# Kernel optimization log

Measured on AMD Instinct MI355X. Metric: run time of the kernel, lower is better.

## Reference

```python
import jax, jax.numpy as jnp
import numpy as np

B, N, D = 256, 512, 128   # meta_batch, num_sample, feat_dim; in_c = 2*D = 256, base_c = 128
EPS_L1 = 1e-12
EPS_BN = 1e-5
NEG_SLOPE = 0.01


def setup_inputs() -> dict:
    key = jax.random.key(0)
    ks = jax.random.split(key, 6)
    return {
        "distribution_edge": jax.random.uniform(ks[0], (B, N, N), dtype=jnp.float32),
        "instance_edge": jax.random.uniform(ks[1], (B, N, N), dtype=jnp.float32),
        "point_node": jax.random.normal(ks[2], (B, N, D), dtype=jnp.float32),
        "W1": jax.random.normal(ks[3], (2 * D, 2 * D), dtype=jnp.float32) * 0.05,  # Conv2d 1x1: (out_c=base_c*2, in_c)
        "g1": jnp.ones((2 * D,), jnp.float32),
        "b1": jnp.zeros((2 * D,), jnp.float32),
        "W2": jax.random.normal(ks[4], (D, 2 * D), dtype=jnp.float32) * 0.05,     # Conv2d 1x1: (out_c=base_c, base_c*2)
        "g2": jnp.ones((D,), jnp.float32),
        "b2": jnp.zeros((D,), jnp.float32),
    }


def _l1_normalize(x):
    # F.normalize(x, p=1, dim=-1): x / max(sum(|x|, -1), 1e-12)
    return x / jnp.clip(jnp.sum(jnp.abs(x), axis=-1, keepdims=True), EPS_L1, None)


def _bn_lrelu(x, g, b):
    # x: (B, C, N); BatchNorm2d training-mode stats over (batch, spatial), biased var
    mean = jnp.mean(x, axis=(0, 2), keepdims=True)
    var = jnp.var(x, axis=(0, 2), keepdims=True)
    y = (x - mean) * jax.lax.rsqrt(var + EPS_BN) * g[None, :, None] + b[None, :, None]
    return jnp.where(y >= 0, y, NEG_SLOPE * y)


def reference(distribution_edge, instance_edge, point_node, W1, g1, b1, W2, g2, b2):
    n = point_node.shape[1]
    diag_mask = 1.0 - jnp.eye(n, dtype=point_node.dtype)  # broadcasts over meta_batch
    edge_feat = _l1_normalize(distribution_edge * diag_mask)
    aggr_feat = jnp.einsum('bij,bjd->bid', edge_feat, point_node)
    edge_instance = _l1_normalize(instance_edge * diag_mask)
    aggr_instance = jnp.einsum('bij,bjd->bid', edge_instance, point_node)
    x = jnp.concatenate([aggr_feat, aggr_instance], axis=-1)  # (B, N, 2D)
    x = jnp.swapaxes(x, 1, 2)                                  # (B, 2D, N)
    h = _bn_lrelu(jnp.einsum('oc,bcn->bon', W1, x), g1, b1)    # 1x1 conv, no bias
    h = _bn_lrelu(jnp.einsum('oc,bcn->bon', W2, h), g2, b2)
    return jnp.swapaxes(h, 1, 2)                               # (B, N, base_c)
```

## Files before the change

kernel.cpp:

```cpp
#include <hip/hip_runtime.h>
#include <hip/hip_bf16.h>
#include <string.h>

#define BB 256
#define NNS 512
#define DDF 128
#define CC1 256
#define CC2 128
#define NPOS (BB * NNS)

typedef __attribute__((ext_vector_type(4))) float f32x4;
typedef __attribute__((ext_vector_type(8))) short bf16x8;

__device__ __forceinline__ short f2bf(float f) {
    __hip_bfloat16 h = __float2bfloat16(f);
    short s;
    __builtin_memcpy(&s, &h, 2);
    return s;
}
__device__ __forceinline__ float bf2f(short s) {
    unsigned int u = ((unsigned int)(unsigned short)s) << 16;
    float f;
    __builtin_memcpy(&f, &u, 4);
    return f;
}

#define MFMA16(a, b, c) __builtin_amdgcn_mfma_f32_16x16x32_bf16(a, b, c, 0, 0, 0)

__global__ void prep_kernel(const float* __restrict__ W1, const float* __restrict__ W2,
                            short* __restrict__ W1b, short* __restrict__ W2b,
                            float* __restrict__ stats) {
    int idx = blockIdx.x * 256 + threadIdx.x;
    if (idx < CC1 * CC1) W1b[idx] = f2bf(W1[idx]);
    if (idx < CC2 * CC1) W2b[idx] = f2bf(W2[idx]);
    if (idx < 1536) stats[idx] = 0.0f;
}

__global__ void transposeP_kernel(const float* __restrict__ P, short* __restrict__ PT) {
    int oid = blockIdx.x * 256 + threadIdx.x;
    int b = oid >> 13;
    int r = oid & 8191;
    int jo = r >> 7;
    int d = r & 127;
    const float* p = P + (size_t)b * (NNS * DDF) + (size_t)(jo * 8) * DDF + d;
    bf16x8 v;
#pragma unroll
    for (int t = 0; t < 8; ++t) v[t] = f2bf(p[t * DDF]);
    *reinterpret_cast<bf16x8*>(PT + ((size_t)(b * DDF + d)) * NNS + jo * 8) = v;
}

__global__ __launch_bounds__(256) void gemm1_kernel(const float* __restrict__ dE,
                                                    const float* __restrict__ iE,
                                                    const short* __restrict__ PT,
                                                    short* __restrict__ X) {
    int bid = blockIdx.x;
    int mtb = bid & 3;
    int e = (bid >> 2) & 1;
    int b = bid >> 3;
    const float* E = (e == 0 ? dE : iE) + (size_t)b * (NNS * NNS);
    const short* PTb = PT + (size_t)b * (DDF * NNS);

    int tid = threadIdx.x;
    int lane = tid & 63, w = tid >> 6;
    int quad = lane >> 4, lr = lane & 15;
    int mh = w >> 1, nh = w & 1;
    int mbase = mtb * 128 + mh * 64;

    f32x4 zero = {0.f, 0.f, 0.f, 0.f};
    f32x4 acc[4][4];
#pragma unroll
    for (int a = 0; a < 4; ++a)
#pragma unroll
        for (int c = 0; c < 4; ++c) acc[a][c] = zero;
    float rs[4] = {0.f, 0.f, 0.f, 0.f};

    for (int kk = 0; kk < 16; ++kk) {
        int k0 = kk * 32 + quad * 8;
        bf16x8 bfr[4];
#pragma unroll
        for (int nt = 0; nt < 4; ++nt) {
            int n = nh * 64 + nt * 16 + lr;
            bfr[nt] = *reinterpret_cast<const bf16x8*>(&PTb[(size_t)n * NNS + k0]);
        }
#pragma unroll
        for (int mt = 0; mt < 4; ++mt) {
            int i = mbase + mt * 16 + lr;
            const float* rp = &E[(size_t)i * NNS + k0];
            float4 v0 = *reinterpret_cast<const float4*>(rp);
            float4 v1 = *reinterpret_cast<const float4*>(rp + 4);
            float a8[8] = {v0.x, v0.y, v0.z, v0.w, v1.x, v1.y, v1.z, v1.w};
#pragma unroll
            for (int t = 0; t < 8; ++t)
                if (k0 + t == i) a8[t] = 0.0f;
#pragma unroll
            for (int t = 0; t < 8; ++t) rs[mt] += fabsf(a8[t]);
            bf16x8 af;
#pragma unroll
            for (int t = 0; t < 8; ++t) af[t] = f2bf(a8[t]);
#pragma unroll
            for (int nt = 0; nt < 4; ++nt) acc[mt][nt] = MFMA16(af, bfr[nt], acc[mt][nt]);
        }
    }

    float inv[4];
#pragma unroll
    for (int mt = 0; mt < 4; ++mt) {
        float s = rs[mt];
        s += __shfl_xor(s, 16, 64);
        s += __shfl_xor(s, 32, 64);
        inv[mt] = 1.0f / fmaxf(s, 1e-12f);
    }
#pragma unroll
    for (int mt = 0; mt < 4; ++mt) {
        float ir[4];
#pragma unroll
        for (int r = 0; r < 4; ++r) ir[r] = __shfl(inv[mt], quad * 4 + r, 64);
#pragma unroll
        for (int nt = 0; nt < 4; ++nt) {
            int col = e * 128 + nh * 64 + nt * 16 + lr;
#pragma unroll
            for (int r = 0; r < 4; ++r) {
                int row = mbase + mt * 16 + quad * 4 + r;
                X[((size_t)b * NNS + row) * CC1 + col] = f2bf(acc[mt][nt][r] * ir[r]);
            }
        }
    }
}

__global__ __launch_bounds__(256) void gemm2_kernel(const short* __restrict__ X,
                                                    const short* __restrict__ W1b,
                                                    short* __restrict__ Y1,
                                                    float* __restrict__ sum1,
                                                    float* __restrict__ sumsq1) {
    int bid = blockIdx.x;
    int ocb = (bid & 1) * 128;
    int pt = bid >> 1;
    int tid = threadIdx.x;
    int lane = tid & 63, w = tid >> 6;
    int quad = lane >> 4, lr = lane & 15;
    int mh = w >> 1, nh = w & 1;
    int pbase = pt * 128 + mh * 64;

    f32x4 zero = {0.f, 0.f, 0.f, 0.f};
    f32x4 acc[4][4];
#pragma unroll
    for (int a = 0; a < 4; ++a)
#pragma unroll
        for (int c = 0; c < 4; ++c) acc[a][c] = zero;

    for (int kk = 0; kk < 8; ++kk) {
        int k0 = kk * 32 + quad * 8;
        bf16x8 bfr[4];
#pragma unroll
        for (int nt = 0; nt < 4; ++nt) {
            int o = ocb + nh * 64 + nt * 16 + lr;
            bfr[nt] = *reinterpret_cast<const bf16x8*>(&W1b[(size_t)o * CC1 + k0]);
        }
#pragma unroll
        for (int mt = 0; mt < 4; ++mt) {
            int pos = pbase + mt * 16 + lr;
            bf16x8 af = *reinterpret_cast<const bf16x8*>(&X[(size_t)pos * CC1 + k0]);
#pragma unroll
            for (int nt = 0; nt < 4; ++nt) acc[mt][nt] = MFMA16(af, bfr[nt], acc[mt][nt]);
        }
    }
#pragma unroll
    for (int nt = 0; nt < 4; ++nt) {
        int o = ocb + nh * 64 + nt * 16 + lr;
        float s = 0.f, q = 0.f;
#pragma unroll
        for (int mt = 0; mt < 4; ++mt)
#pragma unroll
            for (int r = 0; r < 4; ++r) {
                float v = acc[mt][nt][r];
                s += v;
                q += v * v;
            }
        s += __shfl_xor(s, 16, 64); s += __shfl_xor(s, 32, 64);
        q += __shfl_xor(q, 16, 64); q += __shfl_xor(q, 32, 64);
        if (lane < 16) {
            atomicAdd(&sum1[o], s);
            atomicAdd(&sumsq1[o], q);
        }
#pragma unroll
        for (int mt = 0; mt < 4; ++mt)
#pragma unroll
            for (int r = 0; r < 4; ++r) {
                int pos = pbase + mt * 16 + quad * 4 + r;
                Y1[(size_t)pos * CC1 + o] = f2bf(acc[mt][nt][r]);
            }
    }
}

__global__ void finalize_kernel(const float* __restrict__ sum, const float* __restrict__ sumsq,
                                const float* __restrict__ g, const float* __restrict__ b,
                                float* __restrict__ scale, float* __restrict__ shift, int C) {
    int i = threadIdx.x;
    if (i < C) {
        const float invM = 1.0f / (float)NPOS;
        float m = sum[i] * invM;
        float v = sumsq[i] * invM - m * m;
        float s = g[i] * rsqrtf(v + 1e-5f);
        scale[i] = s;
        shift[i] = b[i] - m * s;
    }
}

__global__ __launch_bounds__(256) void gemm3_kernel(const short* __restrict__ Y1,
                                                    const short* __restrict__ W2b,
                                                    const float* __restrict__ scale1,
                                                    const float* __restrict__ shift1,
                                                    float* __restrict__ Y2,
                                                    float* __restrict__ sum2,
                                                    float* __restrict__ sumsq2) {
    __shared__ __align__(16) float ssc[CC1];
    __shared__ __align__(16) float ssh[CC1];
    ssc[threadIdx.x] = scale1[threadIdx.x];
    ssh[threadIdx.x] = shift1[threadIdx.x];
    __syncthreads();

    int pt = blockIdx.x;
    int tid = threadIdx.x;
    int lane = tid & 63, w = tid >> 6;
    int quad = lane >> 4, lr = lane & 15;
    int mh = w >> 1, nh = w & 1;
    int pbase = pt * 128 + mh * 64;

    f32x4 zero = {0.f, 0.f, 0.f, 0.f};
    f32x4 acc[4][4];
#pragma unroll
    for (int a = 0; a < 4; ++a)
#pragma unroll
        for (int c = 0; c < 4; ++c) acc[a][c] = zero;

    for (int kk = 0; kk < 8; ++kk) {
        int k0 = kk * 32 + quad * 8;
        bf16x8 bfr[4];
#pragma unroll
        for (int nt = 0; nt < 4; ++nt) {
            int o = nh * 64 + nt * 16 + lr;
            bfr[nt] = *reinterpret_cast<const bf16x8*>(&W2b[(size_t)o * CC1 + k0]);
        }
        float4 sc0 = *reinterpret_cast<const float4*>(&ssc[k0]);
        float4 sc1 = *reinterpret_cast<const float4*>(&ssc[k0 + 4]);
        float4 sh0 = *reinterpret_cast<const float4*>(&ssh[k0]);
        float4 sh1 = *reinterpret_cast<const float4*>(&ssh[k0 + 4]);
        float scv[8] = {sc0.x, sc0.y, sc0.z, sc0.w, sc1.x, sc1.y, sc1.z, sc1.w};
        float shv[8] = {sh0.x, sh0.y, sh0.z, sh0.w, sh1.x, sh1.y, sh1.z, sh1.w};
#pragma unroll
        for (int mt = 0; mt < 4; ++mt) {
            int pos = pbase + mt * 16 + lr;
            bf16x8 raw = *reinterpret_cast<const bf16x8*>(&Y1[(size_t)pos * CC1 + k0]);
            bf16x8 af;
#pragma unroll
            for (int t = 0; t < 8; ++t) {
                float v = bf2f(raw[t]) * scv[t] + shv[t];
                v = fmaxf(v, 0.01f * v);
                af[t] = f2bf(v);
            }
#pragma unroll
            for (int nt = 0; nt < 4; ++nt) acc[mt][nt] = MFMA16(af, bfr[nt], acc[mt][nt]);
        }
    }
#pragma unroll
    for (int nt = 0; nt < 4; ++nt) {
        int o = nh * 64 + nt * 16 + lr;
        float s = 0.f, q = 0.f;
#pragma unroll
        for (int mt = 0; mt < 4; ++mt)
#pragma unroll
            for (int r = 0; r < 4; ++r) {
                float v = acc[mt][nt][r];
                s += v;
                q += v * v;
            }
        s += __shfl_xor(s, 16, 64); s += __shfl_xor(s, 32, 64);
        q += __shfl_xor(q, 16, 64); q += __shfl_xor(q, 32, 64);
        if (lane < 16) {
            atomicAdd(&sum2[o], s);
            atomicAdd(&sumsq2[o], q);
        }
#pragma unroll
        for (int mt = 0; mt < 4; ++mt)
#pragma unroll
            for (int r = 0; r < 4; ++r) {
                int pos = pbase + mt * 16 + quad * 4 + r;
                Y2[(size_t)pos * CC2 + o] = acc[mt][nt][r];
            }
    }
}

__global__ void apply2_kernel(const float* __restrict__ Y2, const float* __restrict__ scale2,
                              const float* __restrict__ shift2, float* __restrict__ out) {
    size_t gid = (size_t)blockIdx.x * 256 + threadIdx.x;
    size_t base = gid * 4;
    float4 y = *reinterpret_cast<const float4*>(&Y2[base]);
    int o = (int)(base & 127);
    float4 sc = *reinterpret_cast<const float4*>(&scale2[o]);
    float4 sh = *reinterpret_cast<const float4*>(&shift2[o]);
    float4 t;
    t.x = y.x * sc.x + sh.x; t.x = fmaxf(t.x, 0.01f * t.x);
    t.y = y.y * sc.y + sh.y; t.y = fmaxf(t.y, 0.01f * t.y);
    t.z = y.z * sc.z + sh.z; t.z = fmaxf(t.z, 0.01f * t.z);
    t.w = y.w * sc.w + sh.w; t.w = fmaxf(t.w, 0.01f * t.w);
    *reinterpret_cast<float4*>(&out[base]) = t;
}

extern "C" void kernel_launch(void* const* d_in, const int* in_sizes, int n_in,
                              void* d_out, int out_size, void* d_ws, size_t ws_size,
                              hipStream_t stream) {
    const float* dE = (const float*)d_in[0];
    const float* iE = (const float*)d_in[1];
    const float* P  = (const float*)d_in[2];
    const float* W1 = (const float*)d_in[3];
    const float* g1 = (const float*)d_in[4];
    const float* b1 = (const float*)d_in[5];
    const float* W2 = (const float*)d_in[6];
    const float* g2 = (const float*)d_in[7];
    const float* b2 = (const float*)d_in[8];
    float* out = (float*)d_out;
    char* ws = (char*)d_ws;

    short* PT  = (short*)(ws + 0);
    short* X   = (short*)(ws + 33554432);
    short* Y1  = (short*)(ws + 100663296);
    float* Y2  = (float*)(ws + 33554432);
    short* W1b = (short*)(ws + 167772160);
    short* W2b = (short*)(ws + 167903232);
    float* st  = (float*)(ws + 167968768);
    float* sum1 = st,        * sumsq1 = st + 256, * scale1 = st + 512,  * shift1 = st + 768;
    float* sum2 = st + 1024, * sumsq2 = st + 1152, * scale2 = st + 1280, * shift2 = st + 1408;

    prep_kernel<<<256, 256, 0, stream>>>(W1, W2, W1b, W2b, st);
    transposeP_kernel<<<8192, 256, 0, stream>>>(P, PT);
    gemm1_kernel<<<2048, 256, 0, stream>>>(dE, iE, PT, X);
    gemm2_kernel<<<2048, 256, 0, stream>>>(X, W1b, Y1, sum1, sumsq1);
    finalize_kernel<<<1, 256, 0, stream>>>(sum1, sumsq1, g1, b1, scale1, shift1, CC1);
    gemm3_kernel<<<1024, 256, 0, stream>>>(Y1, W2b, scale1, shift1, Y2, sum2, sumsq2);
    finalize_kernel<<<1, 128, 0, stream>>>(sum2, sumsq2, g2, b2, scale2, shift2, CC2);
    apply2_kernel<<<16384, 256, 0, stream>>>(Y2, scale2, shift2, out);
}
```

Before: 893.8 us.

## Stage GEMM A-tiles through LDS with async global_load_lds double buffering

The three GEMM kernels now stream their A operand (edge rows, X, Y1) into XOR-swizzled shared memory with direct global-to-LDS loads, double-buffered across k-steps. Previously each wave read these rows straight from global memory in a strided pattern. The P transpose now goes through an LDS tile so global reads are coalesced. gemm2 moves to 512-thread blocks that cover all 256 output channels, so X is read once per tile instead of twice, and bf16 packing uses paired conversions. The cost is added LDS use and a barrier on every k-step.

```diff
diff --git a/kernel.cpp b/kernel.cpp
--- a/kernel.cpp
+++ b/kernel.cpp
@@ -23,6 +23,19 @@
     float f;
     __builtin_memcpy(&f, &u, 4);
     return f;
+}
+__device__ __forceinline__ unsigned int pk2bf(float a, float b) {
+    float2 t; t.x = a; t.y = b;
+    __hip_bfloat162 h = __float22bfloat162_rn(t);
+    unsigned int u;
+    __builtin_memcpy(&u, &h, 4);
+    return u;
+}
+
+__device__ __forceinline__ void gload_lds16(const void* g, void* l) {
+    __builtin_amdgcn_global_load_lds(
+        (const __attribute__((address_space(1))) unsigned int*)g,
+        (__attribute__((address_space(3))) unsigned int*)l, 16, 0, 0);
 }
 
 #define MFMA16(a, b, c) __builtin_amdgcn_mfma_f32_16x16x32_bf16(a, b, c, 0, 0, 0)
@@ -36,23 +49,37 @@
     if (idx < 1536) stats[idx] = 0.0f;
 }
 
-__global__ void transposeP_kernel(const float* __restrict__ P, short* __restrict__ PT) {
-    int oid = blockIdx.x * 256 + threadIdx.x;
-    int b = oid >> 13;
-    int r = oid & 8191;
-    int jo = r >> 7;
-    int d = r & 127;
-    const float* p = P + (size_t)b * (NNS * DDF) + (size_t)(jo * 8) * DDF + d;
-    bf16x8 v;
-#pragma unroll
-    for (int t = 0; t < 8; ++t) v[t] = f2bf(p[t * DDF]);
-    *reinterpret_cast<bf16x8*>(PT + ((size_t)(b * DDF + d)) * NNS + jo * 8) = v;
+__global__ __launch_bounds__(256) void transposeP_kernel(const float* __restrict__ P,
+                                                         short* __restrict__ PT) {
+    __shared__ float tp[64 * 132];
+    int b = blockIdx.x >> 3;
+    int j0 = (blockIdx.x & 7) * 64;
+    int t = threadIdx.x;
+    const float* Pb = P + ((size_t)b * NNS + j0) * DDF;
+    int jr = t >> 5, dc = (t & 31) * 4;
+#pragma unroll
+    for (int p = 0; p < 8; ++p) {
+        int j = p * 8 + jr;
+        float4 v = *reinterpret_cast<const float4*>(&Pb[(size_t)j * DDF + dc]);
+        *reinterpret_cast<float4*>(&tp[j * 132 + dc]) = v;
+    }
+    __syncthreads();
+    int jo = t & 7;
+#pragma unroll
+    for (int p = 0; p < 4; ++p) {
+        int d = p * 32 + (t >> 3);
+        bf16x8 v;
+#pragma unroll
+        for (int s = 0; s < 8; ++s) v[s] = f2bf(tp[(jo * 8 + s) * 132 + d]);
+        *reinterpret_cast<bf16x8*>(&PT[((size_t)(b * DDF + d)) * NNS + j0 + jo * 8]) = v;
+    }
 }
 
 __global__ __launch_bounds__(256) void gemm1_kernel(const float* __restrict__ dE,
                                                     const float* __restrict__ iE,
                                                     const short* __restrict__ PT,
                                                     short* __restrict__ X) {
+    __shared__ __align__(16) float tA[2][4096];
     int bid = blockIdx.x;
     int mtb = bid & 3;
     int e = (bid >> 2) & 1;
@@ -64,7 +91,16 @@
     int lane = tid & 63, w = tid >> 6;
     int quad = lane >> 4, lr = lane & 15;
     int mh = w >> 1, nh = w & 1;
-    int mbase = mtb * 128 + mh * 64;
+    int mbase = mtb * 128;
+    int mwave = mh * 64;
+
+    int srow[4], scol[4];
+#pragma unroll
+    for (int i = 0; i < 4; ++i) {
+        int rl = i * 32 + (tid >> 3);
+        srow[i] = rl;
+        scol[i] = (tid & 7) ^ (rl & 7);
+    }
 
     f32x4 zero = {0.f, 0.f, 0.f, 0.f};
     f32x4 acc[4][4];
@@ -74,7 +110,22 @@
         for (int c = 0; c < 4; ++c) acc[a][c] = zero;
     float rs[4] = {0.f, 0.f, 0.f, 0.f};
 
+#pragma unroll
+    for (int i = 0; i < 4; ++i)
+        gload_lds16(&E[(size_t)(mbase + srow[i]) * NNS + scol[i] * 4],
+                    (char*)&tA[0][0] + i * 4096 + w * 1024);
+    __syncthreads();
+
     for (int kk = 0; kk < 16; ++kk) {
+        const float* cur = &tA[kk & 1][0];
+        if (kk < 15) {
+            float* nxt = &tA[(kk + 1) & 1][0];
+            int kc = (kk + 1) * 32;
+#pragma unroll
+            for (int i = 0; i < 4; ++i)
+                gload_lds16(&E[(size_t)(mbase + srow[i]) * NNS + kc + scol[i] * 4],
+                            (char*)nxt + i * 4096 + w * 1024);
+        }
         int k0 = kk * 32 + quad * 8;
         bf16x8 bfr[4];
 #pragma unroll
@@ -84,22 +135,26 @@
         }
 #pragma unroll
         for (int mt = 0; mt < 4; ++mt) {
-            int i = mbase + mt * 16 + lr;
-            const float* rp = &E[(size_t)i * NNS + k0];
-            float4 v0 = *reinterpret_cast<const float4*>(rp);
-            float4 v1 = *reinterpret_cast<const float4*>(rp + 4);
+            int rl = mwave + mt * 16 + lr;
+            int i = mbase + rl;
+            int sw = rl & 7;
+            int s0 = rl * 8 + ((quad * 2) ^ sw);
+            int s1 = rl * 8 + ((quad * 2 + 1) ^ sw);
+            float4 v0 = *reinterpret_cast<const float4*>(&cur[s0 * 4]);
+            float4 v1 = *reinterpret_cast<const float4*>(&cur[s1 * 4]);
             float a8[8] = {v0.x, v0.y, v0.z, v0.w, v1.x, v1.y, v1.z, v1.w};
 #pragma unroll
-            for (int t = 0; t < 8; ++t)
-                if (k0 + t == i) a8[t] = 0.0f;
-#pragma unroll
-            for (int t = 0; t < 8; ++t) rs[mt] += fabsf(a8[t]);
-            bf16x8 af;
-#pragma unroll
-            for (int t = 0; t < 8; ++t) af[t] = f2bf(a8[t]);
-#pragma unroll
-            for (int nt = 0; nt < 4; ++nt) acc[mt][nt] = MFMA16(af, bfr[nt], acc[mt][nt]);
-        }
+            for (int tt = 0; tt < 8; ++tt)
+                if (k0 + tt == i) a8[tt] = 0.0f;
+#pragma unroll
+            for (int tt = 0; tt < 8; ++tt) rs[mt] += fabsf(a8[tt]);
+            union { bf16x8 v; unsigned int u[4]; } af;
+#pragma unroll
+            for (int tt = 0; tt < 4; ++tt) af.u[tt] = pk2bf(a8[2 * tt], a8[2 * tt + 1]);
+#pragma unroll
+            for (int nt = 0; nt < 4; ++nt) acc[mt][nt] = MFMA16(af.v, bfr[nt], acc[mt][nt]);
+        }
+        __syncthreads();
     }
 
     float inv[4];
@@ -120,26 +175,29 @@
             int col = e * 128 + nh * 64 + nt * 16 + lr;
 #pragma unroll
             for (int r = 0; r < 4; ++r) {
-                int row = mbase + mt * 16 + quad * 4 + r;
+                int row = mbase + mwave + mt * 16 + quad * 4 + r;
                 X[((size_t)b * NNS + row) * CC1 + col] = f2bf(acc[mt][nt][r] * ir[r]);
             }
         }
     }
 }
 
-__global__ __launch_bounds__(256) void gemm2_kernel(const short* __restrict__ X,
+__global__ __launch_bounds__(512) void gemm2_kernel(const short* __restrict__ X,
                                                     const short* __restrict__ W1b,
                                                     short* __restrict__ Y1,
                                                     float* __restrict__ sum1,
                                                     float* __restrict__ sumsq1) {
-    int bid = blockIdx.x;
-    int ocb = (bid & 1) * 128;
-    int pt = bid >> 1;
+    __shared__ __align__(16) short tA[2][4096];
+    int pbase = blockIdx.x * 128;
     int tid = threadIdx.x;
     int lane = tid & 63, w = tid >> 6;
     int quad = lane >> 4, lr = lane & 15;
-    int mh = w >> 1, nh = w & 1;
-    int pbase = pt * 128 + mh * 64;
+    int mh = w >> 2, nh = w & 3;
+
+    int spair = tid >> 3;
+    int sl3 = (tid & 7) ^ (spair & 7);
+    int srow = spair * 2 + (sl3 >> 2);
+    int scol = sl3 & 3;
 
     f32x4 zero = {0.f, 0.f, 0.f, 0.f};
     f32x4 acc[4][4];
@@ -148,25 +206,36 @@
 #pragma unroll
         for (int c = 0; c < 4; ++c) acc[a][c] = zero;
 
+    gload_lds16(&X[(size_t)(pbase + srow) * CC1 + scol * 8], (char*)&tA[0][0] + w * 1024);
+    __syncthreads();
+
     for (int kk = 0; kk < 8; ++kk) {
+        const short* cur = &tA[kk & 1][0];
+        if (kk < 7)
+            gload_lds16(&X[(size_t)(pbase + srow) * CC1 + (kk + 1) * 32 + scol * 8],
+                        (char*)&tA[(kk + 1) & 1][0] + w * 1024);
         int k0 = kk * 32 + quad * 8;
         bf16x8 bfr[4];
 #pragma unroll
         for (int nt = 0; nt < 4; ++nt) {
-            int o = ocb + nh * 64 + nt * 16 + lr;
+            int o = nh * 64 + nt * 16 + lr;
             bfr[nt] = *reinterpret_cast<const bf16x8*>(&W1b[(size_t)o * CC1 + k0]);
         }
 #pragma unroll
         for (int mt = 0; mt < 4; ++mt) {
-            int pos = pbase + mt * 16 + lr;
-            bf16x8 af = *reinterpret_cast<const bf16x8*>(&X[(size_t)pos * CC1 + k0]);
+            int rl = mh * 64 + mt * 16 + lr;
+            int pair = rl >> 1;
+            int s3 = ((rl & 1) << 2) | quad;
+            int phys = pair * 8 + (s3 ^ (pair & 7));
+            bf16x8 af = *reinterpret_cast<const bf16x8*>(&cur[phys * 8]);
 #pragma unroll
             for (int nt = 0; nt < 4; ++nt) acc[mt][nt] = MFMA16(af, bfr[nt], acc[mt][nt]);
         }
+        __syncthreads();
     }
 #pragma unroll
     for (int nt = 0; nt < 4; ++nt) {
-        int o = ocb + nh * 64 + nt * 16 + lr;
+        int o = nh * 64 + nt * 16 + lr;
         float s = 0.f, q = 0.f;
 #pragma unroll
         for (int mt = 0; mt < 4; ++mt)
@@ -186,7 +255,7 @@
         for (int mt = 0; mt < 4; ++mt)
 #pragma unroll
             for (int r = 0; r < 4; ++r) {
-                int pos = pbase + mt * 16 + quad * 4 + r;
+                int pos = pbase + mh * 64 + mt * 16 + quad * 4 + r;
                 Y1[(size_t)pos * CC1 + o] = f2bf(acc[mt][nt][r]);
             }
     }
@@ -213,18 +282,27 @@
                                                     float* __restrict__ Y2,
                                                     float* __restrict__ sum2,
                                                     float* __restrict__ sumsq2) {
+    __shared__ __align__(16) short tA[2][4096];
     __shared__ __align__(16) float ssc[CC1];
     __shared__ __align__(16) float ssh[CC1];
     ssc[threadIdx.x] = scale1[threadIdx.x];
     ssh[threadIdx.x] = shift1[threadIdx.x];
-    __syncthreads();
-
-    int pt = blockIdx.x;
+
+    int pbase = blockIdx.x * 128;
     int tid = threadIdx.x;
     int lane = tid & 63, w = tid >> 6;
     int quad = lane >> 4, lr = lane & 15;
     int mh = w >> 1, nh = w & 1;
-    int pbase = pt * 128 + mh * 64;
+
+    int srow[2], scol[2];
+#pragma unroll
+    for (int i = 0; i < 2; ++i) {
+        int slot = i * 256 + tid;
+        int pair = slot >> 3;
+        int s3 = (slot & 7) ^ (pair & 7);
+        srow[i] = pair * 2 + (s3 >> 2);
+        scol[i] = s3 & 3;
+    }
 
     f32x4 zero = {0.f, 0.f, 0.f, 0.f};
     f32x4 acc[4][4];
@@ -233,7 +311,20 @@
 #pragma unroll
         for (int c = 0; c < 4; ++c) acc[a][c] = zero;
 
+#pragma unroll
+    for (int i = 0; i < 2; ++i)
+        gload_lds16(&Y1[(size_t)(pbase + srow[i]) * CC1 + scol[i] * 8],
+                    (char*)&tA[0][0] + i * 4096 + w * 1024);
+    __syncthreads();
+
     for (int kk = 0; kk < 8; ++kk) {
+        const short* cur = &tA[kk & 1][0];
+        if (kk < 7) {
+#pragma unroll
+            for (int i = 0; i < 2; ++i)
+                gload_lds16(&Y1[(size_t)(pbase + srow[i]) * CC1 + (kk + 1) * 32 + scol[i] * 8],
+                            (char*)&tA[(kk + 1) & 1][0] + i * 4096 + w * 1024);
+        }
         int k0 = kk * 32 + quad * 8;
         bf16x8 bfr[4];
 #pragma unroll
@@ -249,18 +340,24 @@
         float shv[8] = {sh0.x, sh0.y, sh0.z, sh0.w, sh1.x, sh1.y, sh1.z, sh1.w};
 #pragma unroll
         for (int mt = 0; mt < 4; ++mt) {
-            int pos = pbase + mt * 16 + lr;
-            bf16x8 raw = *reinterpret_cast<const bf16x8*>(&Y1[(size_t)pos * CC1 + k0]);
-            bf16x8 af;
-#pragma unroll
-            for (int t = 0; t < 8; ++t) {
-                float v = bf2f(raw[t]) * scv[t] + shv[t];
-                v = fmaxf(v, 0.01f * v);
-                af[t] = f2bf(v);
-            }
-#pragma unroll
-            for (int nt = 0; nt < 4; ++nt) acc[mt][nt] = MFMA16(af, bfr[nt], acc[mt][nt]);
-        }
+            int rl = mh * 64 + mt * 16 + lr;
+            int pair = rl >> 1;
+            int s3 = ((rl & 1) << 2) | quad;
+            int phys = pair * 8 + (s3 ^ (pair & 7));
+            bf16x8 raw = *reinterpret_cast<const bf16x8*>(&cur[phys * 8]);
+            union { bf16x8 v; unsigned int u[4]; } af;
+#pragma unroll
+            for (int tt = 0; tt < 4; ++tt) {
+                float va = bf2f(raw[2 * tt]) * scv[2 * tt] + shv[2 * tt];
+                va = fmaxf(va, 0.01f * va);
+                float vb = bf2f(raw[2 * tt + 1]) * scv[2 * tt + 1] + shv[2 * tt + 1];
+                vb = fmaxf(vb, 0.01f * vb);
+                af.u[tt] = pk2bf(va, vb);
+            }
+#pragma unroll
+            for (int nt = 0; nt < 4; ++nt) acc[mt][nt] = MFMA16(af.v, bfr[nt], acc[mt][nt]);
+        }
+        __syncthreads();
     }
 #pragma unroll
     for (int nt = 0; nt < 4; ++nt) {
@@ -284,7 +381,7 @@
         for (int mt = 0; mt < 4; ++mt)
 #pragma unroll
             for (int r = 0; r < 4; ++r) {
-                int pos = pbase + mt * 16 + quad * 4 + r;
+                int pos = pbase + mh * 64 + mt * 16 + quad * 4 + r;
                 Y2[(size_t)pos * CC2 + o] = acc[mt][nt][r];
             }
     }
@@ -332,9 +429,9 @@
     float* sum2 = st + 1024, * sumsq2 = st + 1152, * scale2 = st + 1280, * shift2 = st + 1408;
 
     prep_kernel<<<256, 256, 0, stream>>>(W1, W2, W1b, W2b, st);
-    transposeP_kernel<<<8192, 256, 0, stream>>>(P, PT);
+    transposeP_kernel<<<2048, 256, 0, stream>>>(P, PT);
     gemm1_kernel<<<2048, 256, 0, stream>>>(dE, iE, PT, X);
-    gemm2_kernel<<<2048, 256, 0, stream>>>(X, W1b, Y1, sum1, sumsq1);
+    gemm2_kernel<<<1024, 512, 0, stream>>>(X, W1b, Y1, sum1, sumsq1);
     finalize_kernel<<<1, 256, 0, stream>>>(sum1, sumsq1, g1, b1, scale1, shift1, CC1);
     gemm3_kernel<<<1024, 256, 0, stream>>>(Y1, W2b, scale1, shift1, Y2, sum2, sumsq2);
     finalize_kernel<<<1, 128, 0, stream>>>(sum2, sumsq2, g2, b2, scale2, shift2, CC2);
```

New measurement: 783.6 us. 1.14x faster.
